# Kernel optimization log

Measured on AMD Instinct MI355X. Metric: run time of the kernel, lower is better.

Reference implementation:

```python
import jax, jax.numpy as jnp
import numpy as np

N_BITS = 4
GROUP_SIZE = 128
CLIP_RATIO = 1.0  # no clipping when == 1.0
EPS = 1e-5


def setup_inputs() -> dict:
    key = jax.random.key(0)
    k1, k2 = jax.random.split(key)
    B, S, C = 4, 4096, 4096
    x = jax.random.normal(k1, (B, S, C), dtype=jnp.float32)
    perm = jax.random.permutation(k2, C).astype(jnp.int32)
    inv = jnp.argsort(perm).astype(jnp.int32)
    return {"x": x, "perm_indices": perm, "inverse_perm_indices": inv}


def _quantize_groupwise(w):
    """Asymmetric int quant/dequant, quant_method='max', per flat group of GROUP_SIZE."""
    saved_shape = w.shape
    g = w.reshape(-1, GROUP_SIZE)  # [num_groups, group_size]
    q_max = 2 ** N_BITS - 1  # asym: q_min = 0
    w_max = jnp.max(g, axis=-1, keepdims=True)
    w_min = jnp.min(g, axis=-1, keepdims=True)
    scales = jnp.clip(w_max - w_min, EPS, None) / q_max
    base = jnp.clip(jnp.round(-w_min / scales), 0, q_max)
    q = (jnp.clip(jnp.round(g / scales) + base, 0, q_max) - base) * scales
    return q.reshape(saved_shape)


def reference(x, perm_indices, inverse_perm_indices):
    # cluster-based channel permutation -> group-wise quant/dequant -> inverse permutation
    x_perm = jnp.take(x, perm_indices, axis=-1)
    x_q = _quantize_groupwise(x_perm)
    return jnp.take(x_q, inverse_perm_indices, axis=-1)
```

## Files before the change

kernel.cpp:

```cpp
#include <hip/hip_runtime.h>
#include <stdint.h>


constexpr int C     = 4096;
constexpr int GS    = 128;
constexpr int NG    = C / GS;
constexpr int BLOCK = 512;
constexpr int WAVES = BLOCK / 64;
constexpr int GPW   = NG / WAVES;
constexpr int VECS  = C / 4 / BLOCK;

typedef const __attribute__((address_space(1))) uint32_t glb_u32;
typedef __attribute__((address_space(3))) uint32_t lds_u32;

__device__ __forceinline__ void stage_row(const float* __restrict__ src,
                                          float* dst, int wave, int lane) {
    #pragma unroll
    for (int i = 0; i < 2; ++i) {
        const float* g = src + i * 2048 + wave * 256 + lane * 4;
        float*       l = dst + i * 2048 + wave * 256;
        __builtin_amdgcn_global_load_lds((glb_u32*)(uintptr_t)g,
                                         (lds_u32*)(uintptr_t)l, 16, 0, 0);
    }
}

__global__ __launch_bounds__(BLOCK, 8) void tpq_kernel(
    const float* __restrict__ x,
    const int*   __restrict__ gat,
    const int*   __restrict__ asn,
    float*       __restrict__ out,
    int rows)
{
    __shared__ float  rowbuf[2][C];
    __shared__ float2 sb[NG];

    const int tid  = threadIdx.x;
    const int wave = tid >> 6;
    const int lane = tid & 63;

    int pidx0[GPW], pidx1[GPW];
    #pragma unroll
    for (int gi = 0; gi < GPW; ++gi) {
        const int g = wave * GPW + gi;
        pidx0[gi] = gat[g * GS + lane];
        pidx1[gi] = gat[g * GS + 64 + lane];
    }
    uint32_t gpack[VECS];
    #pragma unroll
    for (int i = 0; i < VECS; ++i) {
        const int4 a = reinterpret_cast<const int4*>(asn)[tid + i * BLOCK];
        gpack[i] = (uint32_t)(a.x >> 7)        | ((uint32_t)(a.y >> 7) << 8)
                 | ((uint32_t)(a.z >> 7) << 16) | ((uint32_t)(a.w >> 7) << 24);
    }

    int r = blockIdx.x;
    if (r >= rows) return;
    stage_row(x + (size_t)r * C, rowbuf[0], wave, lane);
    int cur = 0;

    while (true) {
        __syncthreads();
        const int  rn = r + gridDim.x;
        const bool hn = rn < rows;
        if (hn) stage_row(x + (size_t)rn * C, rowbuf[cur ^ 1], wave, lane);

        const float* rc = rowbuf[cur];
        #pragma unroll
        for (int gi = 0; gi < GPW; ++gi) {
            const float v0 = rc[pidx0[gi]];
            const float v1 = rc[pidx1[gi]];
            float mx = fmaxf(v0, v1);
            float mn = fminf(v0, v1);
            #pragma unroll
            for (int off = 32; off; off >>= 1) {
                mx = fmaxf(mx, __shfl_xor(mx, off));
                mn = fminf(mn, __shfl_xor(mn, off));
            }
            if (lane == 0) {
                const float s = fmaxf(mx - mn, 1e-5f) * (1.0f / 15.0f);
                const float b = fminf(fmaxf(rintf(-mn / s), 0.0f), 15.0f);
                sb[wave * GPW + gi] = make_float2(s, b);
            }
        }
        __syncthreads();

        const float4* rc4 = reinterpret_cast<const float4*>(rc);
        float4*       or4 = reinterpret_cast<float4*>(out + (size_t)r * C);
        #pragma unroll
        for (int i = 0; i < VECS; ++i) {
            const float4   v  = rc4[tid + i * BLOCK];
            const uint32_t gp = gpack[i];
            float4 o;
            { const float2 p = sb[gp & 31u];
              o.x = (fminf(fmaxf(rintf(v.x / p.x) + p.y, 0.0f), 15.0f) - p.y) * p.x; }
            { const float2 p = sb[(gp >> 8) & 31u];
              o.y = (fminf(fmaxf(rintf(v.y / p.x) + p.y, 0.0f), 15.0f) - p.y) * p.x; }
            { const float2 p = sb[(gp >> 16) & 31u];
              o.z = (fminf(fmaxf(rintf(v.z / p.x) + p.y, 0.0f), 15.0f) - p.y) * p.x; }
            { const float2 p = sb[(gp >> 24) & 31u];
              o.w = (fminf(fmaxf(rintf(v.w / p.x) + p.y, 0.0f), 15.0f) - p.y) * p.x; }
            or4[tid + i * BLOCK] = o;
        }

        if (!hn) break;
        r = rn;
        cur ^= 1;
    }
}

extern "C" void kernel_launch(void* const* d_in, const int* in_sizes, int n_in,
                              void* d_out, int out_size, void* d_ws, size_t ws_size,
                              hipStream_t stream) {
    const float* x   = (const float*)d_in[0];
    const int*   gat = (const int*)d_in[1];
    const int*   asn = (const int*)d_in[2];
    float* out = (float*)d_out;

    const int rows = in_sizes[0] / C;
    const int nblk = rows < 2048 ? rows : 2048;

    tpq_kernel<<<nblk, BLOCK, 0, stream>>>(x, gat, asn, out, rows);
}
```

Measured before the change: 118.7 us.

## Replace LDS DMA double-buffering with register prefetch and 16-lane group reductions

Drops the async global_load_lds double-buffered row staging in favour of prefetching the next row into registers, then writing it into a single LDS row buffer once the current row's output is done. Block size goes from 512 to 256 threads. Each group's min/max is now computed by a 16-lane subgroup, each lane covering 8 permuted elements, with gather indices read as int4 from global memory every row instead of being held in registers. The quantize pass reads values from registers rather than LDS, and raw s_barrier asm replaces __syncthreads. This trades LDS traffic and barrier count for register pressure and repeated index loads, and the runtime swap of pointers into local arrays may push those arrays into scratch memory.

Result: slower. 209.7 us (+76.6%).

```diff
diff --git a/kernel.cpp b/kernel.cpp
--- a/kernel.cpp
+++ b/kernel.cpp
@@ -5,24 +5,10 @@
 constexpr int C     = 4096;
 constexpr int GS    = 128;
 constexpr int NG    = C / GS;
-constexpr int BLOCK = 512;
-constexpr int WAVES = BLOCK / 64;
-constexpr int GPW   = NG / WAVES;
+constexpr int BLOCK = 256;
 constexpr int VECS  = C / 4 / BLOCK;
-
-typedef const __attribute__((address_space(1))) uint32_t glb_u32;
-typedef __attribute__((address_space(3))) uint32_t lds_u32;
-
-__device__ __forceinline__ void stage_row(const float* __restrict__ src,
-                                          float* dst, int wave, int lane) {
-    #pragma unroll
-    for (int i = 0; i < 2; ++i) {
-        const float* g = src + i * 2048 + wave * 256 + lane * 4;
-        float*       l = dst + i * 2048 + wave * 256;
-        __builtin_amdgcn_global_load_lds((glb_u32*)(uintptr_t)g,
-                                         (lds_u32*)(uintptr_t)l, 16, 0, 0);
-    }
-}
+constexpr int NSG   = BLOCK / 16;
+constexpr int GPS   = NG / NSG;
 
 __global__ __launch_bounds__(BLOCK, 8) void tpq_kernel(
     const float* __restrict__ x,
@@ -31,20 +17,17 @@
     float*       __restrict__ out,
     int rows)
 {
-    __shared__ float  rowbuf[2][C];
+    __shared__ float  rowbuf[C];
     __shared__ float2 sb[NG];
 
     const int tid  = threadIdx.x;
     const int wave = tid >> 6;
     const int lane = tid & 63;
+    const int sg   = wave * 4 + (lane >> 4);
+    const int sl   = lane & 15;
 
-    int pidx0[GPW], pidx1[GPW];
-    #pragma unroll
-    for (int gi = 0; gi < GPW; ++gi) {
-        const int g = wave * GPW + gi;
-        pidx0[gi] = gat[g * GS + lane];
-        pidx1[gi] = gat[g * GS + 64 + lane];
-    }
+    float4* rw4 = reinterpret_cast<float4*>(rowbuf);
+
     uint32_t gpack[VECS];
     #pragma unroll
     for (int i = 0; i < VECS; ++i) {
@@ -54,41 +37,61 @@
     }
 
     int r = blockIdx.x;
-    if (r >= rows) return;
-    stage_row(x + (size_t)r * C, rowbuf[0], wave, lane);
-    int cur = 0;
+    float4 va[VECS], vb[VECS];
+
+    {
+        const float4* x4 = reinterpret_cast<const float4*>(x + (size_t)r * C);
+        #pragma unroll
+        for (int i = 0; i < VECS; ++i) va[i] = x4[tid + i * BLOCK];
+        #pragma unroll
+        for (int i = 0; i < VECS; ++i) rw4[tid + i * BLOCK] = va[i];
+        __syncthreads();
+    }
+
+    float4* vcur = va;
+    float4* vnxt = vb;
 
     while (true) {
-        __syncthreads();
         const int  rn = r + gridDim.x;
         const bool hn = rn < rows;
-        if (hn) stage_row(x + (size_t)rn * C, rowbuf[cur ^ 1], wave, lane);
 
-        const float* rc = rowbuf[cur];
+        if (hn) {
+            const float4* nx4 = reinterpret_cast<const float4*>(x + (size_t)rn * C);
+            #pragma unroll
+            for (int i = 0; i < VECS; ++i) vnxt[i] = nx4[tid + i * BLOCK];
+        }
+
         #pragma unroll
-        for (int gi = 0; gi < GPW; ++gi) {
-            const float v0 = rc[pidx0[gi]];
-            const float v1 = rc[pidx1[gi]];
-            float mx = fmaxf(v0, v1);
-            float mn = fminf(v0, v1);
+        for (int gi = 0; gi < GPS; ++gi) {
+            const int g = sg * GPS + gi;
+            const int4* gp4 = reinterpret_cast<const int4*>(gat + g * GS + sl * 8);
+            const int4 ia = gp4[0], ib = gp4[1];
+            const float x0 = rowbuf[ia.x], x1 = rowbuf[ia.y];
+            const float x2 = rowbuf[ia.z], x3 = rowbuf[ia.w];
+            const float x4v = rowbuf[ib.x], x5 = rowbuf[ib.y];
+            const float x6 = rowbuf[ib.z], x7 = rowbuf[ib.w];
+            float mx = fmaxf(fmaxf(fmaxf(x0, x1), fmaxf(x2, x3)),
+                             fmaxf(fmaxf(x4v, x5), fmaxf(x6, x7)));
+            float mn = fminf(fminf(fminf(x0, x1), fminf(x2, x3)),
+                             fminf(fminf(x4v, x5), fminf(x6, x7)));
             #pragma unroll
-            for (int off = 32; off; off >>= 1) {
+            for (int off = 8; off; off >>= 1) {
                 mx = fmaxf(mx, __shfl_xor(mx, off));
                 mn = fminf(mn, __shfl_xor(mn, off));
             }
-            if (lane == 0) {
+            if (sl == 0) {
                 const float s = fmaxf(mx - mn, 1e-5f) * (1.0f / 15.0f);
                 const float b = fminf(fmaxf(rintf(-mn / s), 0.0f), 15.0f);
-                sb[wave * GPW + gi] = make_float2(s, b);
+                sb[g] = make_float2(s, b);
             }
         }
-        __syncthreads();
 
-        const float4* rc4 = reinterpret_cast<const float4*>(rc);
-        float4*       or4 = reinterpret_cast<float4*>(out + (size_t)r * C);
+        asm volatile("s_waitcnt lgkmcnt(0)\n\ts_barrier" ::: "memory");
+
+        float4* or4 = reinterpret_cast<float4*>(out + (size_t)r * C);
         #pragma unroll
         for (int i = 0; i < VECS; ++i) {
-            const float4   v  = rc4[tid + i * BLOCK];
+            const float4   v  = vcur[i];
             const uint32_t gp = gpack[i];
             float4 o;
             { const float2 p = sb[gp & 31u];
@@ -103,8 +106,13 @@
         }
 
         if (!hn) break;
+
+        #pragma unroll
+        for (int i = 0; i < VECS; ++i) rw4[tid + i * BLOCK] = vnxt[i];
+        asm volatile("s_waitcnt lgkmcnt(0)\n\ts_barrier" ::: "memory");
+
         r = rn;
-        cur ^= 1;
+        float4* t = vcur; vcur = vnxt; vnxt = t;
     }
 }
 
```
